# Optimization experiments

Measured on AMD Instinct MI355X. Metric: run time of the kernel, lower is better.

The kernel has to match this reference:

```python
import jax, jax.numpy as jnp
import numpy as np

BS, SEQ, H, OUT = 32, 64, 256, 1

def setup_inputs() -> dict:
    key = jax.random.key(0)
    ks = jax.random.split(key, 8)
    s3 = 1.0 / np.sqrt(3 * H)
    sh = 1.0 / np.sqrt(H)
    x = jax.random.normal(ks[0], (BS, SEQ, H), dtype=jnp.float32)
    # ChaoticAttention: Linear(3H -> H) scoring, softmax over seq
    Wa = jax.random.normal(ks[1], (3 * H, H), dtype=jnp.float32) * s3
    ba = jnp.zeros((H,), dtype=jnp.float32)
    # ChaoticLSTM cell: gates = context @ Wi + ht @ Wh + b, order i,f,g,o
    Wi = jax.random.normal(ks[2], (H, 4 * H), dtype=jnp.float32) * sh
    Wh = jax.random.normal(ks[3], (H, 4 * H), dtype=jnp.float32) * sh
    b = jnp.zeros((4 * H,), dtype=jnp.float32)
    # final fc: Linear(H -> OUT)
    Wf = jax.random.normal(ks[4], (H, OUT), dtype=jnp.float32) * sh
    bf = jnp.zeros((OUT,), dtype=jnp.float32)
    return {"x": x, "Wa": Wa, "ba": ba, "Wi": Wi, "Wh": Wh, "b": b, "Wf": Wf, "bf": bf}

def reference(x, Wa, ba, Wi, Wh, b, Wf, bf):
    bs, seq, hid = x.shape

    def step(carry, _):
        ht, ct = carry
        # attention over the full input sequence conditioned on (ht, ct)
        hrep = jnp.broadcast_to(ht[:, None, :], (bs, seq, hid))
        crep = jnp.broadcast_to(ct[:, None, :], (bs, seq, hid))
        feat = jnp.concatenate([x, hrep, crep], axis=-1)          # (bs, seq, 3H)
        alpha = jax.nn.softmax(feat @ Wa + ba, axis=1)            # softmax over seq
        context = jnp.sum(alpha * x, axis=1)                      # (bs, H)
        # one LSTM cell step on the context vector
        gates = context @ Wi + ht @ Wh + b                        # (bs, 4H)
        i, f, g, o = jnp.split(gates, 4, axis=-1)
        ct_new = jax.nn.sigmoid(f) * ct + jax.nn.sigmoid(i) * jnp.tanh(g)
        ht_new = jax.nn.sigmoid(o) * jnp.tanh(ct_new)
        return (ht_new, ct_new), None

    h0 = jnp.zeros((bs, hid), dtype=x.dtype)
    c0 = jnp.zeros((bs, hid), dtype=x.dtype)
    (ht, ct), _ = jax.lax.scan(step, (h0, c0), None, length=seq)
    return ht @ Wf + bf                                           # (bs, OUT)
```

## Files before the change

### kernel.cpp

```cpp
#include <hip/hip_runtime.h>

#define BSZ   32
#define SEQ   64
#define HID   256
#define G4    1024
#define NSTEP 64
#define QB    8
#define JB    32

typedef unsigned long long u64;
typedef unsigned int       u32;

__device__ __forceinline__ float sigmoidf_(float v) { return 1.f / (1.f + __expf(-v)); }

__global__ __launch_bounds__(256, 1) void k_fused(
    const float* __restrict__ x, const float* __restrict__ Wa,
    const float* __restrict__ Wi, const float* __restrict__ Wh,
    const float* __restrict__ bias, const float* __restrict__ Wf,
    const float* __restrict__ bf,
    u64* __restrict__ tht, u64* __restrict__ ctxT, float* __restrict__ out)
{
  const int b    = blockIdx.x >> 3;
  const int q    = blockIdx.x & 7;
  const int tid  = threadIdx.x;
  const int lane = tid & 63;
  const int wv   = tid >> 6;
  const int jj   = tid & 31;
  const int kq   = tid >> 5;
  const int qj   = q * JB + jj;

  __shared__ __align__(16) float arena[32768];
  __shared__ __align__(16) float hs[256];
  __shared__ __align__(16) float cs[256];
  __shared__ __align__(16) float gred[2][8][JB * 4];
  __shared__ float red[4];

  const float* xb = x + (size_t)b * SEQ * HID;

#pragma unroll
  for (int it = 0; it < 16; ++it) {
    const int g = it * 1024 + tid * 4;
    const int s = g >> 8, k = g & 255;
    *(float4*)&arena[s * 260 + k] = *(const float4*)(xb + g);
  }
#pragma unroll
  for (int it = 0; it < 8; ++it) {
    const int idx = it * 256 + tid;
    const int k = idx >> 3, cq = idx & 7;
    *(float4*)&arena[16640 + k * 32 + cq * 4] =
        *(const float4*)(Wa + (size_t)k * HID + q * JB + cq * 4);
  }
  __syncthreads();

  {
    const int ts = tid >> 2, tc = tid & 3;
    float l0 = 0.f, l1 = 0.f, l2 = 0.f, l3 = 0.f,
          l4 = 0.f, l5 = 0.f, l6 = 0.f, l7 = 0.f;
    const float* xrow = &arena[ts * 260];
    const float* wab  = &arena[16640 + tc * 8];
    for (int k4 = 0; k4 < 64; ++k4) {
      const float4 xv = *(const float4*)&xrow[k4 * 4];
#define LSTEP(XE, KO)                                                        \
      { const float4 wa = *(const float4*)&wab[(k4 * 4 + KO) * 32];          \
        const float4 wb2 = *(const float4*)&wab[(k4 * 4 + KO) * 32 + 4];     \
        l0 += (XE) * wa.x;  l1 += (XE) * wa.y;  l2 += (XE) * wa.z;           \
        l3 += (XE) * wa.w;  l4 += (XE) * wb2.x; l5 += (XE) * wb2.y;          \
        l6 += (XE) * wb2.z; l7 += (XE) * wb2.w; }
      LSTEP(xv.x, 0) LSTEP(xv.y, 1) LSTEP(xv.z, 2) LSTEP(xv.w, 3)
#undef LSTEP
    }
    float* lrow = &arena[24832 + ts * 33 + tc * 8];
    lrow[0] = l0; lrow[1] = l1; lrow[2] = l2; lrow[3] = l3;
    lrow[4] = l4; lrow[5] = l5; lrow[6] = l6; lrow[7] = l7;
  }
  __syncthreads();

  {
    const int jx = tid >> 3, sp = tid & 7;
    float lg[8];
#pragma unroll
    for (int e = 0; e < 8; ++e) lg[e] = arena[24832 + (sp * 8 + e) * 33 + jx];
    float m = lg[0];
#pragma unroll
    for (int e = 1; e < 8; ++e) m = fmaxf(m, lg[e]);
    m = fmaxf(m, __shfl_xor(m, 1));
    m = fmaxf(m, __shfl_xor(m, 2));
    m = fmaxf(m, __shfl_xor(m, 4));
    float ex[8], sm = 0.f;
#pragma unroll
    for (int e = 0; e < 8; ++e) { ex[e] = __expf(lg[e] - m); sm += ex[e]; }
    sm += __shfl_xor(sm, 1);
    sm += __shfl_xor(sm, 2);
    sm += __shfl_xor(sm, 4);
    const float inv = 1.f / sm;
    const int gj = q * JB + jx;
    float cx = 0.f;
#pragma unroll
    for (int e = 0; e < 8; ++e) cx += ex[e] * arena[(sp * 8 + e) * 260 + gj];
    cx *= inv;
    cx += __shfl_xor(cx, 1);
    cx += __shfl_xor(cx, 2);
    cx += __shfl_xor(cx, 4);
    if (sp == 0)
      __hip_atomic_store(ctxT + b * HID + gj,
                         (((u64)__float_as_uint(cx)) << 32) | 1ull,
                         __ATOMIC_RELAXED, __HIP_MEMORY_SCOPE_AGENT);
  }
  __syncthreads();

#define MAC32(HSRC, ACC)                                                     \
  _Pragma("unroll")                                                          \
  for (int ks4 = 0; ks4 < 8; ++ks4) {                                        \
    const float4 h4 = *(const float4*)&(HSRC)[kq * 32 + ks4 * 4];            \
    _Pragma("unroll")                                                        \
    for (int e = 0; e < 4; ++e) {                                            \
      const float he = (e == 0) ? h4.x : (e == 1) ? h4.y                     \
                     : (e == 2) ? h4.z : h4.w;                               \
      const float* wrow = &arena[(kq * 32 + ks4 * 4 + e) * 128];             \
      ACC.x += he * wrow[jj];                                                \
      ACC.y += he * wrow[32 + jj];                                           \
      ACC.z += he * wrow[64 + jj];                                           \
      ACC.w += he * wrow[96 + jj];                                           \
    }                                                                        \
  }

#pragma unroll
  for (int i = 0; i < 32; ++i) {
    const int f = i * 256 + tid;
    const int k = f >> 5, c4 = f & 31;
    const int g = c4 >> 3, jw = c4 & 7;
    *(float4*)&arena[f * 4] =
        *(const float4*)(Wi + (size_t)k * G4 + g * HID + q * JB + jw * 4);
  }
  {
    const u64* pp = ctxT + b * HID + tid;
    u64 pk;
    do {
      pk = __hip_atomic_load(pp, __ATOMIC_RELAXED, __HIP_MEMORY_SCOPE_AGENT);
    } while ((u32)pk != 1u);
    cs[tid] = __uint_as_float((u32)(pk >> 32));
  }
  __syncthreads();

  float4 ac = {0.f, 0.f, 0.f, 0.f};
  MAC32(cs, ac);
  *(float4*)&gred[0][kq][jj * 4] = ac;
  __syncthreads();

  float4 gcr = {0.f, 0.f, 0.f, 0.f};
  float  cst = 0.f;
  if (tid < 32) {
#pragma unroll
    for (int k2 = 0; k2 < 8; ++k2) {
      const float4 v = *(const float4*)&gred[0][k2][tid * 4];
      gcr.x += v.x; gcr.y += v.y; gcr.z += v.z; gcr.w += v.w;
    }
    gcr.x += bias[qj];           gcr.y += bias[HID + qj];
    gcr.z += bias[2 * HID + qj]; gcr.w += bias[3 * HID + qj];
    const float ig = sigmoidf_(gcr.x), fg0 = sigmoidf_(gcr.y);
    const float gg = tanhf(gcr.z),     og  = sigmoidf_(gcr.w);
    (void)fg0;
    cst = ig * gg;
    const float hv = og * tanhf(cst);
    __hip_atomic_store(tht + (size_t)1 * BSZ * HID + (size_t)b * HID + qj,
                       (((u64)__float_as_uint(hv)) << 32) | 1ull,
                       __ATOMIC_RELAXED, __HIP_MEMORY_SCOPE_AGENT);
  }
#pragma unroll
  for (int i = 0; i < 32; ++i) {
    const int f = i * 256 + tid;
    const int k = f >> 5, c4 = f & 31;
    const int g = c4 >> 3, jw = c4 & 7;
    *(float4*)&arena[f * 4] =
        *(const float4*)(Wh + (size_t)k * G4 + g * HID + q * JB + jw * 4);
  }
  __syncthreads();

  for (int t = 1; t < NSTEP; ++t) {
    const int rb = t & 1;
    {
      const u64* pp = tht + (size_t)rb * BSZ * HID + (size_t)b * HID + tid;
      u64 pk;
      do {
        pk = __hip_atomic_load(pp, __ATOMIC_RELAXED, __HIP_MEMORY_SCOPE_AGENT);
      } while ((u32)pk != (u32)t);
      hs[tid] = __uint_as_float((u32)(pk >> 32));
    }
    float4 a2 = {0.f, 0.f, 0.f, 0.f};
    MAC32(hs, a2);
    *(float4*)&gred[rb][kq][jj * 4] = a2;
    __syncthreads();

    if (tid < 32) {
      float4 s = gcr;
#pragma unroll
      for (int k2 = 0; k2 < 8; ++k2) {
        const float4 v = *(const float4*)&gred[rb][k2][tid * 4];
        s.x += v.x; s.y += v.y; s.z += v.z; s.w += v.w;
      }
      const float ig = sigmoidf_(s.x), fg = sigmoidf_(s.y);
      const float gg = tanhf(s.z),     og = sigmoidf_(s.w);
      cst = fg * cst + ig * gg;
      const float hv = og * tanhf(cst);
      __hip_atomic_store(tht + (size_t)((t + 1) & 1) * BSZ * HID
                             + (size_t)b * HID + qj,
                         (((u64)__float_as_uint(hv)) << 32) | (u64)(u32)(t + 1),
                         __ATOMIC_RELAXED, __HIP_MEMORY_SCOPE_AGENT);
    }
  }

  if (q == 0) {
    const u64* pp = tht +  (size_t)b * HID + tid;
    u64 pk;
    do {
      pk = __hip_atomic_load(pp, __ATOMIC_RELAXED, __HIP_MEMORY_SCOPE_AGENT);
    } while ((u32)pk != (u32)NSTEP);
    const float hv = __uint_as_float((u32)(pk >> 32));
    float prod = hv * Wf[tid];
#pragma unroll
    for (int mk = 1; mk < 64; mk <<= 1) prod += __shfl_xor(prod, mk);
    if (lane == 0) red[wv] = prod;
    __syncthreads();
    if (tid == 0) out[b] = red[0] + red[1] + red[2] + red[3] + bf[0];
  }
#undef MAC32
}

extern "C" void kernel_launch(void* const* d_in, const int* in_sizes, int n_in,
                              void* d_out, int out_size, void* d_ws, size_t ws_size,
                              hipStream_t stream)
{
  const float* x  = (const float*)d_in[0];
  const float* Wa = (const float*)d_in[1];
  const float* Wi = (const float*)d_in[3];
  const float* Wh = (const float*)d_in[4];
  const float* bi = (const float*)d_in[5];
  const float* Wf = (const float*)d_in[6];
  const float* bf = (const float*)d_in[7];
  float* out = (float*)d_out;

  u64* tht  = (u64*)d_ws;
  u64* ctxT = (u64*)((char*)d_ws + 2 * BSZ * HID * sizeof(u64));

  hipLaunchKernelGGL(k_fused, dim3(BSZ * QB), dim3(256), 0, stream,
                     x, Wa, Wi, Wh, bi, Wf, bf, tht, ctxT, out);
}
```

Before: 194.2 us.

## Vectorize recurrent MAC with float4 weight loads and remap block-to-batch order

The LDS matrix-vector product in the recurrent step now has each thread read four contiguous columns of one gate as float4, instead of four scalar loads strided across gates. This cuts the number of LDS instructions per step. The gate-reduction indexing changes to match the new output layout. Block indexing also swaps so that consecutive blocks take different batches rather than different column slices of one batch, which changes how the cooperating blocks are placed across XCDs and may alter the latency of the cross-block spin-wait.

```diff
diff --git a/kernel.cpp b/kernel.cpp
--- a/kernel.cpp
+++ b/kernel.cpp
@@ -20,14 +20,14 @@
     const float* __restrict__ bf,
     u64* __restrict__ tht, u64* __restrict__ ctxT, float* __restrict__ out)
 {
-  const int b    = blockIdx.x >> 3;
-  const int q    = blockIdx.x & 7;
+  const int b    = blockIdx.x & 31;
+  const int q    = blockIdx.x >> 5;
   const int tid  = threadIdx.x;
   const int lane = tid & 63;
   const int wv   = tid >> 6;
-  const int jj   = tid & 31;
+  const int jq   = tid & 7;
+  const int g    = (tid >> 3) & 3;
   const int kq   = tid >> 5;
-  const int qj   = q * JB + jj;
 
   __shared__ __align__(16) float arena[32768];
   __shared__ __align__(16) float hs[256];
@@ -39,9 +39,9 @@
 
 #pragma unroll
   for (int it = 0; it < 16; ++it) {
-    const int g = it * 1024 + tid * 4;
-    const int s = g >> 8, k = g & 255;
-    *(float4*)&arena[s * 260 + k] = *(const float4*)(xb + g);
+    const int gl = it * 1024 + tid * 4;
+    const int s = gl >> 8, k = gl & 255;
+    *(float4*)&arena[s * 260 + k] = *(const float4*)(xb + gl);
   }
 #pragma unroll
   for (int it = 0; it < 8; ++it) {
@@ -110,27 +110,26 @@
 
 #define MAC32(HSRC, ACC)                                                     \
   _Pragma("unroll")                                                          \
-  for (int ks4 = 0; ks4 < 8; ++ks4) {                                        \
-    const float4 h4 = *(const float4*)&(HSRC)[kq * 32 + ks4 * 4];            \
-    _Pragma("unroll")                                                        \
-    for (int e = 0; e < 4; ++e) {                                            \
-      const float he = (e == 0) ? h4.x : (e == 1) ? h4.y                     \
-                     : (e == 2) ? h4.z : h4.w;                               \
-      const float* wrow = &arena[(kq * 32 + ks4 * 4 + e) * 128];             \
-      ACC.x += he * wrow[jj];                                                \
-      ACC.y += he * wrow[32 + jj];                                           \
-      ACC.z += he * wrow[64 + jj];                                           \
-      ACC.w += he * wrow[96 + jj];                                           \
-    }                                                                        \
+  for (int k4 = 0; k4 < 8; ++k4) {                                           \
+    const float4 h4 = *(const float4*)&(HSRC)[kq * 32 + k4 * 4];             \
+    const float* wp = &arena[(kq * 32 + k4 * 4) * 128 + g * 32 + jq * 4];    \
+    const float4 w0 = *(const float4*)&wp[0];                                \
+    const float4 w1 = *(const float4*)&wp[128];                              \
+    const float4 w2 = *(const float4*)&wp[256];                              \
+    const float4 w3 = *(const float4*)&wp[384];                              \
+    ACC.x += h4.x * w0.x + h4.y * w1.x + h4.z * w2.x + h4.w * w3.x;          \
+    ACC.y += h4.x * w0.y + h4.y * w1.y + h4.z * w2.y + h4.w * w3.y;          \
+    ACC.z += h4.x * w0.z + h4.y * w1.z + h4.z * w2.z + h4.w * w3.z;          \
+    ACC.w += h4.x * w0.w + h4.y * w1.w + h4.z * w2.w + h4.w * w3.w;          \
   }
 
 #pragma unroll
   for (int i = 0; i < 32; ++i) {
     const int f = i * 256 + tid;
     const int k = f >> 5, c4 = f & 31;
-    const int g = c4 >> 3, jw = c4 & 7;
+    const int gq = c4 >> 3, jw = c4 & 7;
     *(float4*)&arena[f * 4] =
-        *(const float4*)(Wi + (size_t)k * G4 + g * HID + q * JB + jw * 4);
+        *(const float4*)(Wi + (size_t)k * G4 + gq * HID + q * JB + jw * 4);
   }
   {
     const u64* pp = ctxT + b * HID + tid;
@@ -144,22 +143,22 @@
 
   float4 ac = {0.f, 0.f, 0.f, 0.f};
   MAC32(cs, ac);
-  *(float4*)&gred[0][kq][jj * 4] = ac;
+  *(float4*)&gred[0][kq][g * 32 + jq * 4] = ac;
   __syncthreads();
 
   float4 gcr = {0.f, 0.f, 0.f, 0.f};
   float  cst = 0.f;
   if (tid < 32) {
+    const int qj = q * JB + tid;
 #pragma unroll
     for (int k2 = 0; k2 < 8; ++k2) {
-      const float4 v = *(const float4*)&gred[0][k2][tid * 4];
-      gcr.x += v.x; gcr.y += v.y; gcr.z += v.z; gcr.w += v.w;
+      const float* gp = &gred[0][k2][tid];
+      gcr.x += gp[0]; gcr.y += gp[32]; gcr.z += gp[64]; gcr.w += gp[96];
     }
     gcr.x += bias[qj];           gcr.y += bias[HID + qj];
     gcr.z += bias[2 * HID + qj]; gcr.w += bias[3 * HID + qj];
-    const float ig = sigmoidf_(gcr.x), fg0 = sigmoidf_(gcr.y);
-    const float gg = tanhf(gcr.z),     og  = sigmoidf_(gcr.w);
-    (void)fg0;
+    const float ig = sigmoidf_(gcr.x);
+    const float gg = tanhf(gcr.z), og = sigmoidf_(gcr.w);
     cst = ig * gg;
     const float hv = og * tanhf(cst);
     __hip_atomic_store(tht + (size_t)1 * BSZ * HID + (size_t)b * HID + qj,
@@ -170,9 +169,9 @@
   for (int i = 0; i < 32; ++i) {
     const int f = i * 256 + tid;
     const int k = f >> 5, c4 = f & 31;
-    const int g = c4 >> 3, jw = c4 & 7;
+    const int gq = c4 >> 3, jw = c4 & 7;
     *(float4*)&arena[f * 4] =
-        *(const float4*)(Wh + (size_t)k * G4 + g * HID + q * JB + jw * 4);
+        *(const float4*)(Wh + (size_t)k * G4 + gq * HID + q * JB + jw * 4);
   }
   __syncthreads();
 
@@ -188,22 +187,22 @@
     }
     float4 a2 = {0.f, 0.f, 0.f, 0.f};
     MAC32(hs, a2);
-    *(float4*)&gred[rb][kq][jj * 4] = a2;
+    *(float4*)&gred[rb][kq][g * 32 + jq * 4] = a2;
     __syncthreads();
 
     if (tid < 32) {
       float4 s = gcr;
 #pragma unroll
       for (int k2 = 0; k2 < 8; ++k2) {
-        const float4 v = *(const float4*)&gred[rb][k2][tid * 4];
-        s.x += v.x; s.y += v.y; s.z += v.z; s.w += v.w;
+        const float* gp = &gred[rb][k2][tid];
+        s.x += gp[0]; s.y += gp[32]; s.z += gp[64]; s.w += gp[96];
       }
       const float ig = sigmoidf_(s.x), fg = sigmoidf_(s.y);
       const float gg = tanhf(s.z),     og = sigmoidf_(s.w);
       cst = fg * cst + ig * gg;
       const float hv = og * tanhf(cst);
       __hip_atomic_store(tht + (size_t)((t + 1) & 1) * BSZ * HID
-                             + (size_t)b * HID + qj,
+                             + (size_t)b * HID + q * JB + tid,
                          (((u64)__float_as_uint(hv)) << 32) | (u64)(u32)(t + 1),
                          __ATOMIC_RELAXED, __HIP_MEMORY_SCOPE_AGENT);
     }
```

After: 159.2 us. 18.0% less time.
